# Optimization experiments

Measured on AMD Instinct MI355X. Metric: run time of the kernel, lower is better.

## Reference

```python
import jax, jax.numpy as jnp
import numpy as np

D_MODEL = 1024
NUM_HEADS = 16
HEAD_DIM = D_MODEL // NUM_HEADS  # 64
ROPE_THETA = 10000.0
BATCH = 2
SEQ = 2048
NEG_INF = -1e30


def setup_inputs() -> dict:
    key = jax.random.key(0)
    ks = jax.random.split(key, 6)
    std = 1.0 / np.sqrt(D_MODEL)
    x = jax.random.normal(ks[0], (BATCH, SEQ, D_MODEL), dtype=jnp.float32)
    wq = jax.random.normal(ks[1], (D_MODEL, D_MODEL), dtype=jnp.float32) * std
    wk = jax.random.normal(ks[2], (D_MODEL, D_MODEL), dtype=jnp.float32) * std
    wv = jax.random.normal(ks[3], (D_MODEL, D_MODEL), dtype=jnp.float32) * std
    wo = jax.random.normal(ks[4], (D_MODEL, D_MODEL), dtype=jnp.float32) * std
    token_positions = jnp.broadcast_to(jnp.arange(SEQ, dtype=jnp.int32)[None, :], (BATCH, SEQ))
    return {"x": x, "token_positions": token_positions, "wq": wq, "wk": wk, "wv": wv, "wo": wo}


def _apply_rope(t, token_positions):
    # t: (B, H, S, head_dim), token_positions: (B, S)
    half = HEAD_DIM // 2
    inv_freq = 1.0 / (ROPE_THETA ** (2.0 * jnp.arange(half, dtype=jnp.float32) / HEAD_DIM))
    angles = token_positions.astype(jnp.float32)[..., None] * inv_freq  # (B, S, half)
    cos = jnp.cos(angles)[:, None, :, :]  # (B, 1, S, half)
    sin = jnp.sin(angles)[:, None, :, :]
    tp = t.reshape(*t.shape[:-1], half, 2)  # interleaved pairs
    x1, x2 = tp[..., 0], tp[..., 1]
    r1 = x1 * cos - x2 * sin
    r2 = x1 * sin + x2 * cos
    return jnp.stack([r1, r2], axis=-1).reshape(t.shape)


def reference(x, token_positions, wq, wk, wv, wo):
    B, S, D = x.shape
    H, hd = NUM_HEADS, HEAD_DIM
    # projections (Linear: y = x @ W.T, no bias)
    q = (x @ wq.T).reshape(B, S, H, hd).transpose(0, 2, 1, 3)  # (B, H, S, hd)
    k = (x @ wk.T).reshape(B, S, H, hd).transpose(0, 2, 1, 3)
    v = (x @ wv.T).reshape(B, S, H, hd).transpose(0, 2, 1, 3)
    # RoPE on Q, K
    q = _apply_rope(q, token_positions)
    k = _apply_rope(k, token_positions)
    # causal scaled dot-product attention
    scores = jnp.einsum("bhqd,bhkd->bhqk", q, k) / jnp.sqrt(jnp.float32(hd))
    mask = jnp.tril(jnp.ones((S, S), dtype=bool))
    scores = jnp.where(mask, scores, NEG_INF)
    probs = jax.nn.softmax(scores, axis=-1)
    attn = jnp.einsum("bhqk,bhkd->bhqd", probs, v)  # (B, H, S, hd)
    attn = attn.transpose(0, 2, 1, 3).reshape(B, S, D)
    return attn @ wo.T
```

## Files before the change

kernel.cpp:

```cpp
#include <hip/hip_runtime.h>
#include <stdint.h>
#include <math.h>

#define SEQ 2048
#define NH 16
#define DM 1024

typedef __bf16 bf16x8 __attribute__((ext_vector_type(8)));
typedef float f32x4 __attribute__((ext_vector_type(4)));

__device__ __forceinline__ unsigned short f2bf(float f) {
  union { float f; unsigned u; } v; v.f = f;
  unsigned r = v.u + 0x7fffu + ((v.u >> 16) & 1u);
  return (unsigned short)(r >> 16);
}
__device__ __forceinline__ unsigned pk2(float a, float b) {
  return (unsigned)f2bf(a) | ((unsigned)f2bf(b) << 16);
}
__device__ __forceinline__ void load_lds16(const void* g, void* l) {
  __builtin_amdgcn_global_load_lds((__attribute__((address_space(1))) void*)g,
                                   (__attribute__((address_space(3))) void*)l,
                                   16, 0, 0);
}

__global__ void cvt_all(const float* __restrict__ x, const float* __restrict__ wq,
                        const float* __restrict__ wk, const float* __restrict__ wv,
                        const float* __restrict__ wo, unsigned short* __restrict__ ws) {
  const int i = blockIdx.x * blockDim.x + threadIdx.x;
  const int off = i * 4;
  const float* src;
  unsigned short* dst;
  if (off < 4194304) {
    src = x + off;  dst = ws + off;
  } else {
    const int r = off - 4194304;
    const int w = r >> 20, o = r & 1048575;
    const float* tabs[4] = {wq, wk, wv, wo};
    src = tabs[w] + o;  dst = ws + 4194304 + (w << 20) + o;
  }
  const float4 v = *(const float4*)src;
  ushort4 u;
  u.x = f2bf(v.x); u.y = f2bf(v.y); u.z = f2bf(v.z); u.w = f2bf(v.w);
  *(ushort4*)dst = u;
}

__launch_bounds__(256, 2)
__global__ void gemm_qkv(const unsigned short* __restrict__ X,
                         const unsigned short* __restrict__ W3,
                         unsigned short* __restrict__ Qr,
                         unsigned short* __restrict__ Kr,
                         unsigned short* __restrict__ Vt,
                         const int* __restrict__ tp) {
  __shared__ __align__(16) char smem[16384];
  char* As = smem;
  char* Bs = smem + 8192;

  const int t = threadIdx.x;
  const int lane = t & 63, wave = t >> 6;
  const int quad = lane >> 4, l16 = lane & 15;
  const int m0 = blockIdx.y * 128, n0 = blockIdx.x * 128;
  const int wm = (wave >> 1) * 64, wn = (wave & 1) * 64;

  f32x4 acc[4][4];
#pragma unroll
  for (int i = 0; i < 4; i++)
#pragma unroll
    for (int j = 0; j < 4; j++) { acc[i][j][0]=0.f; acc[i][j][1]=0.f; acc[i][j][2]=0.f; acc[i][j][3]=0.f; }

  const int rr = t >> 2;
  const int cc = (t & 3) * 8;

  for (int k0 = 0; k0 < 1024; k0 += 32) {
    __syncthreads();
#pragma unroll
    for (int i = 0; i < 2; i++) {
      load_lds16(X  + (uint64_t)(m0 + i * 64 + rr) * 1024 + k0 + cc, As + i * 4096 + wave * 1024);
      load_lds16(W3 + (uint64_t)(n0 + i * 64 + rr) * 1024 + k0 + cc, Bs + i * 4096 + wave * 1024);
    }
    __syncthreads();

    bf16x8 af[4], bfr[4];
#pragma unroll
    for (int i = 0; i < 4; i++) {
      af[i]  = *(const bf16x8*)(As + (wm + i * 16 + l16) * 64 + quad * 16);
      bfr[i] = *(const bf16x8*)(Bs + (wn + i * 16 + l16) * 64 + quad * 16);
    }
#pragma unroll
    for (int i = 0; i < 4; i++)
#pragma unroll
      for (int j = 0; j < 4; j++)
        acc[i][j] = __builtin_amdgcn_mfma_f32_16x16x32_bf16(af[i], bfr[j], acc[i][j], 0, 0, 0);
  }

  if (n0 < 2048) {
    unsigned short* dst = (n0 < 1024) ? Qr : Kr;
    float fr[4]; int dd[4], hh[4];
#pragma unroll
    for (int j = 0; j < 4; j++) {
      const int n = n0 + wn + j * 16 + l16;
      dd[j] = n & 63;
      hh[j] = (n & 1023) >> 6;
      fr[j] = __builtin_amdgcn_exp2f(-0.20762050594f * (float)(dd[j] & ~1)) * 0.15915494309f;
    }
    const float sgnodd = (l16 & 1) ? 1.f : -1.f;
#pragma unroll
    for (int i = 0; i < 4; i++) {
#pragma unroll
      for (int r = 0; r < 4; r++) {
        const int m = m0 + wm + i * 16 + quad * 4 + r;
        const int s = m & 2047, b = m >> 11;
        const float posf = (float)tp[m];
#pragma unroll
        for (int j = 0; j < 4; j++) {
          const float v = acc[i][j][r];
          const float p = __shfl_xor(v, 1);
          float rev = posf * fr[j];
          rev -= floorf(rev);
          float sn, cs;
          asm("v_sin_f32 %0, %1" : "=v"(sn) : "v"(rev));
          asm("v_cos_f32 %0, %1" : "=v"(cs) : "v"(rev));
          const float rv = fmaf(v, cs, p * sn * sgnodd);
          dst[((uint64_t)((b * NH + hh[j]) * SEQ + s)) * 64 + dd[j]] = f2bf(rv);
        }
      }
    }
  } else {
#pragma unroll
    for (int i = 0; i < 4; i++) {
      const int m = m0 + wm + i * 16 + quad * 4;
      const int s = m & 2047, b = m >> 11;
#pragma unroll
      for (int j = 0; j < 4; j++) {
        const int n = n0 - 2048 + wn + j * 16 + l16;
        const int h = n >> 6, d = n & 63;
        uint2 w;
        w.x = pk2(acc[i][j][0], acc[i][j][1]);
        w.y = pk2(acc[i][j][2], acc[i][j][3]);
        *(uint2*)(Vt + ((uint64_t)((b * NH + h) * 64 + d)) * SEQ + s) = w;
      }
    }
  }
}

__launch_bounds__(256, 2)
__global__ void gemm_ao(const unsigned short* __restrict__ A,
                        const unsigned short* __restrict__ B,
                        float* __restrict__ C) {
  __shared__ __align__(16) char smem[12288];
  char* As = smem;
  char* Bs = smem + 8192;

  const int t = threadIdx.x;
  const int lane = t & 63, wave = t >> 6;
  const int quad = lane >> 4, l16 = lane & 15;
  const int m0 = blockIdx.y * 128, n0 = blockIdx.x * 64;
  const int wm = (wave >> 1) * 64, wn = (wave & 1) * 32;

  f32x4 acc[4][2];
#pragma unroll
  for (int i = 0; i < 4; i++)
#pragma unroll
    for (int j = 0; j < 2; j++) { acc[i][j][0]=0.f; acc[i][j][1]=0.f; acc[i][j][2]=0.f; acc[i][j][3]=0.f; }

  const int rr = t >> 2;
  const int cc = (t & 3) * 8;

  for (int k0 = 0; k0 < 1024; k0 += 32) {
    __syncthreads();
#pragma unroll
    for (int i = 0; i < 2; i++)
      load_lds16(A + (uint64_t)(m0 + i * 64 + rr) * 1024 + k0 + cc, As + i * 4096 + wave * 1024);
    load_lds16(B + (uint64_t)(n0 + rr) * 1024 + k0 + cc, Bs + wave * 1024);
    __syncthreads();

    bf16x8 af[4], bfr[2];
#pragma unroll
    for (int i = 0; i < 4; i++)
      af[i] = *(const bf16x8*)(As + (wm + i * 16 + l16) * 64 + quad * 16);
#pragma unroll
    for (int j = 0; j < 2; j++)
      bfr[j] = *(const bf16x8*)(Bs + (wn + j * 16 + l16) * 64 + quad * 16);
#pragma unroll
    for (int i = 0; i < 4; i++)
#pragma unroll
      for (int j = 0; j < 2; j++)
        acc[i][j] = __builtin_amdgcn_mfma_f32_16x16x32_bf16(af[i], bfr[j], acc[i][j], 0, 0, 0);
  }

#pragma unroll
  for (int i = 0; i < 4; i++)
#pragma unroll
    for (int j = 0; j < 2; j++)
#pragma unroll
      for (int r = 0; r < 4; r++) {
        const int m = m0 + wm + i * 16 + quad * 4 + r;
        const int n = n0 + wn + j * 16 + l16;
        C[(uint64_t)m * DM + n] = acc[i][j][r];
      }
}

__launch_bounds__(256, 4)
__global__ void flash_attn(const unsigned short* __restrict__ Q,
                           const unsigned short* __restrict__ K,
                           const unsigned short* __restrict__ Vt,
                           unsigned short* __restrict__ Oa) {
  __shared__ __align__(16) char smem[40960];

  const int t = threadIdx.x;
  const int lane = t & 63, wave = t >> 6;
  const int quad = lane >> 4, l16 = lane & 15;
  const int bx = blockIdx.x;
  const int qt = (bx & 1) ? (31 - (bx >> 1)) : (bx >> 1);
  const int bh = blockIdx.y;
  const int qbase = qt * 64;
  const uint64_t base = (uint64_t)bh * (SEQ * 64);
  const int qg = qbase + wave * 16 + l16;

  bf16x8 qf[2];
  {
    const unsigned short* qp = Q + base + (uint64_t)qg * 64 + quad * 8;
    qf[0] = *(const bf16x8*)qp;
    qf[1] = *(const bf16x8*)(qp + 32);
  }

  f32x4 o[4];
#pragma unroll
  for (int i = 0; i < 4; i++) { o[i][0]=0.f; o[i][1]=0.f; o[i][2]=0.f; o[i][3]=0.f; }
  float mI = -1e30f, lI = 0.f;

  const int srow = wave * 8 + (lane >> 3);
  const int sc = ((lane & 7) ^ (lane >> 3)) * 8;
  const int swz = (l16 & 7);
  char* ps = smem + 32768 + wave * 2048;

#define STAGE(bufidx, kb_) do {                                                   \
    char* kd_ = smem + (bufidx) * 8192;                                           \
    char* vd_ = smem + 16384 + (bufidx) * 8192;                                   \
    _Pragma("unroll")                                                             \
    for (int i_ = 0; i_ < 2; i_++) {                                              \
      load_lds16(K  + base + (uint64_t)((kb_) + i_ * 32 + srow) * 64 + sc,        \
                 kd_ + i_ * 4096 + wave * 1024);                                  \
      load_lds16(Vt + base + (uint64_t)(i_ * 32 + srow) * SEQ + (kb_) + sc,       \
                 vd_ + i_ * 4096 + wave * 1024);                                  \
    }                                                                             \
  } while (0)

  STAGE(0, 0);

  for (int kt = 0; kt <= qt; kt++) {
    const int kb = kt * 64;
    const int buf = kt & 1;
    __syncthreads();
    if (kt < qt) STAGE(buf ^ 1, kb + 64);
    char* ks = smem + buf * 8192;
    char* vs = smem + 16384 + buf * 8192;
    const bool diag = (kt == qt);
    const int nbmax = diag ? (wave + 1) : 4;

    f32x4 sf[4];
#pragma unroll
    for (int nb = 0; nb < 4; nb++) {
      if (nb < nbmax) {
        f32x4 s; s[0]=0.f; s[1]=0.f; s[2]=0.f; s[3]=0.f;
#pragma unroll
        for (int kk = 0; kk < 2; kk++) {
          bf16x8 kfr = *(const bf16x8*)(ks + (nb * 16 + l16) * 128 + (((kk * 4 + quad) ^ swz) * 16));
          s = __builtin_amdgcn_mfma_f32_16x16x32_bf16(kfr, qf[kk], s, 0, 0, 0);
        }
        sf[nb] = s;
      } else {
        sf[nb][0] = -1e30f; sf[nb][1] = -1e30f; sf[nb][2] = -1e30f; sf[nb][3] = -1e30f;
      }
    }
    if (diag) {
#pragma unroll
      for (int nb = 0; nb < 4; nb++)
#pragma unroll
        for (int r = 0; r < 4; r++)
          if (kb + nb * 16 + quad * 4 + r > qg) sf[nb][r] = -1e30f;
    }

    float mx = sf[0][0];
#pragma unroll
    for (int nb = 0; nb < 4; nb++)
#pragma unroll
      for (int r = 0; r < 4; r++) mx = fmaxf(mx, sf[nb][r]);
    mx = fmaxf(mx, __shfl_xor(mx, 16));
    mx = fmaxf(mx, __shfl_xor(mx, 32));
    const float mnew = fmaxf(mI, mx);
    const float c1 = 0.18033688011f;
    const float mc = mnew * c1;
    const float alpha = __builtin_amdgcn_exp2f(mI * c1 - mc);
    mI = mnew;
    float ls = 0.f;
#pragma unroll
    for (int nb = 0; nb < 4; nb++)
#pragma unroll
      for (int r = 0; r < 4; r++) {
        const float p = __builtin_amdgcn_exp2f(sf[nb][r] * c1 - mc);
        sf[nb][r] = p;
        ls += p;
      }
    lI = lI * alpha + ls;
#pragma unroll
    for (int db = 0; db < 4; db++)
#pragma unroll
      for (int r = 0; r < 4; r++) o[db][r] *= alpha;

#pragma unroll
    for (int nb = 0; nb < 4; nb++) {
      uint2 pv;
      pv.x = pk2(sf[nb][0], sf[nb][1]);
      pv.y = pk2(sf[nb][2], sf[nb][3]);
      *(uint2*)(ps + l16 * 128 + (((nb * 2 + (quad >> 1)) ^ swz) * 16) + (quad & 1) * 8) = pv;
    }

    const int kkmax = diag ? ((wave >> 1) + 1) : 2;
    for (int kk = 0; kk < kkmax; kk++) {
      bf16x8 pf = *(const bf16x8*)(ps + l16 * 128 + (((kk * 4 + quad) ^ swz) * 16));
#pragma unroll
      for (int db = 0; db < 4; db++) {
        bf16x8 vf = *(const bf16x8*)(vs + (db * 16 + l16) * 128 + (((kk * 4 + quad) ^ swz) * 16));
        o[db] = __builtin_amdgcn_mfma_f32_16x16x32_bf16(vf, pf, o[db], 0, 0, 0);
      }
    }
  }
#undef STAGE

  lI += __shfl_xor(lI, 16);
  lI += __shfl_xor(lI, 32);
  const float invl = 1.0f / lI;
  const int b = bh >> 4, h = bh & 15;
  unsigned short* orow = Oa + ((uint64_t)(b * SEQ + qg)) * DM + h * 64 + quad * 4;
#pragma unroll
  for (int db = 0; db < 4; db++) {
    uint2 w;
    w.x = pk2(o[db][0] * invl, o[db][1] * invl);
    w.y = pk2(o[db][2] * invl, o[db][3] * invl);
    *(uint2*)(orow + db * 16) = w;
  }
}

extern "C" void kernel_launch(void* const* d_in, const int* in_sizes, int n_in,
                              void* d_out, int out_size, void* d_ws, size_t ws_size,
                              hipStream_t stream) {
  const float* x  = (const float*)d_in[0];
  const int* tp   = (const int*)d_in[1];
  const float* wq = (const float*)d_in[2];
  const float* wk = (const float*)d_in[3];
  const float* wv = (const float*)d_in[4];
  const float* wo = (const float*)d_in[5];
  float* out = (float*)d_out;

  unsigned short* ws = (unsigned short*)d_ws;
  unsigned short* xb  = ws;
  unsigned short* w3b = ws + 4194304;
  unsigned short* wob = ws + 7340032;
  unsigned short* Qr  = ws + 8388608;
  unsigned short* Kr  = ws + 12582912;
  unsigned short* Vt  = ws + 16777216;
  unsigned short* At  = ws + 20971520;

  cvt_all<<<8192, 256, 0, stream>>>(x, wq, wk, wv, wo, ws);
  gemm_qkv<<<dim3(24, 32), 256, 0, stream>>>(xb, w3b, Qr, Kr, Vt, tp);
  flash_attn<<<dim3(32, 32), 256, 0, stream>>>(Qr, Kr, Vt, At);
  gemm_ao<<<dim3(16, 32), 256, 0, stream>>>(At, wob, out);
}
```

Baseline: 206.5 us.

## Double-buffer LDS tiles in projection GEMMs and use raw waitcnt+barrier

Both GEMM kernels now use two LDS buffers so the async global-to-LDS load of the next K-slice is issued before computing on the current one, cutting the main loop to one barrier per iteration. The __syncthreads calls are replaced with an explicit s_waitcnt vmcnt(0) plus s_barrier, including in flash attention. This hides global load latency behind MFMA work. The cost is twice the LDS per block, which may lower occupancy, and correctness now depends on the hand-written waits covering the direct-to-LDS loads.

New measurement: 207.0 us. Within noise of the previous version (+0.3%).

```diff
diff --git a/kernel.cpp b/kernel.cpp
--- a/kernel.cpp
+++ b/kernel.cpp
@@ -8,6 +8,9 @@
 
 typedef __bf16 bf16x8 __attribute__((ext_vector_type(8)));
 typedef float f32x4 __attribute__((ext_vector_type(4)));
+
+#define ASM_VMCNT0  asm volatile("s_waitcnt vmcnt(0)" ::: "memory")
+#define ASM_BARRIER asm volatile("s_barrier" ::: "memory")
 
 __device__ __forceinline__ unsigned short f2bf(float f) {
   union { float f; unsigned u; } v; v.f = f;
@@ -51,9 +54,7 @@
                          unsigned short* __restrict__ Kr,
                          unsigned short* __restrict__ Vt,
                          const int* __restrict__ tp) {
-  __shared__ __align__(16) char smem[16384];
-  char* As = smem;
-  char* Bs = smem + 8192;
+  __shared__ __align__(16) char smem[32768];
 
   const int t = threadIdx.x;
   const int lane = t & 63, wave = t >> 6;
@@ -70,14 +71,27 @@
   const int rr = t >> 2;
   const int cc = (t & 3) * 8;
 
+#define QKV_STAGE(bufidx, k0_) do {                                               \
+    char* a_ = smem + (bufidx) * 8192;                                            \
+    char* b_ = smem + 16384 + (bufidx) * 8192;                                    \
+    _Pragma("unroll")                                                             \
+    for (int i_ = 0; i_ < 2; i_++) {                                              \
+      load_lds16(X  + (uint64_t)(m0 + i_ * 64 + rr) * 1024 + (k0_) + cc,          \
+                 a_ + i_ * 4096 + wave * 1024);                                   \
+      load_lds16(W3 + (uint64_t)(n0 + i_ * 64 + rr) * 1024 + (k0_) + cc,          \
+                 b_ + i_ * 4096 + wave * 1024);                                   \
+    }                                                                             \
+  } while (0)
+
+  QKV_STAGE(0, 0);
+
   for (int k0 = 0; k0 < 1024; k0 += 32) {
-    __syncthreads();
-#pragma unroll
-    for (int i = 0; i < 2; i++) {
-      load_lds16(X  + (uint64_t)(m0 + i * 64 + rr) * 1024 + k0 + cc, As + i * 4096 + wave * 1024);
-      load_lds16(W3 + (uint64_t)(n0 + i * 64 + rr) * 1024 + k0 + cc, Bs + i * 4096 + wave * 1024);
-    }
-    __syncthreads();
+    const int buf = (k0 >> 5) & 1;
+    ASM_VMCNT0;
+    ASM_BARRIER;
+    if (k0 + 32 < 1024) QKV_STAGE(buf ^ 1, k0 + 32);
+    char* As = smem + buf * 8192;
+    char* Bs = smem + 16384 + buf * 8192;
 
     bf16x8 af[4], bfr[4];
 #pragma unroll
@@ -91,6 +105,7 @@
       for (int j = 0; j < 4; j++)
         acc[i][j] = __builtin_amdgcn_mfma_f32_16x16x32_bf16(af[i], bfr[j], acc[i][j], 0, 0, 0);
   }
+#undef QKV_STAGE
 
   if (n0 < 2048) {
     unsigned short* dst = (n0 < 1024) ? Qr : Kr;
@@ -146,9 +161,7 @@
 __global__ void gemm_ao(const unsigned short* __restrict__ A,
                         const unsigned short* __restrict__ B,
                         float* __restrict__ C) {
-  __shared__ __align__(16) char smem[12288];
-  char* As = smem;
-  char* Bs = smem + 8192;
+  __shared__ __align__(16) char smem[24576];
 
   const int t = threadIdx.x;
   const int lane = t & 63, wave = t >> 6;
@@ -165,13 +178,25 @@
   const int rr = t >> 2;
   const int cc = (t & 3) * 8;
 
+#define AO_STAGE(bufidx, k0_) do {                                                \
+    char* a_ = smem + (bufidx) * 8192;                                            \
+    char* b_ = smem + 16384 + (bufidx) * 4096;                                    \
+    _Pragma("unroll")                                                             \
+    for (int i_ = 0; i_ < 2; i_++)                                                \
+      load_lds16(A + (uint64_t)(m0 + i_ * 64 + rr) * 1024 + (k0_) + cc,           \
+                 a_ + i_ * 4096 + wave * 1024);                                   \
+    load_lds16(B + (uint64_t)(n0 + rr) * 1024 + (k0_) + cc, b_ + wave * 1024);    \
+  } while (0)
+
+  AO_STAGE(0, 0);
+
   for (int k0 = 0; k0 < 1024; k0 += 32) {
-    __syncthreads();
-#pragma unroll
-    for (int i = 0; i < 2; i++)
-      load_lds16(A + (uint64_t)(m0 + i * 64 + rr) * 1024 + k0 + cc, As + i * 4096 + wave * 1024);
-    load_lds16(B + (uint64_t)(n0 + rr) * 1024 + k0 + cc, Bs + wave * 1024);
-    __syncthreads();
+    const int buf = (k0 >> 5) & 1;
+    ASM_VMCNT0;
+    ASM_BARRIER;
+    if (k0 + 32 < 1024) AO_STAGE(buf ^ 1, k0 + 32);
+    char* As = smem + buf * 8192;
+    char* Bs = smem + 16384 + buf * 4096;
 
     bf16x8 af[4], bfr[2];
 #pragma unroll
@@ -186,6 +211,7 @@
       for (int j = 0; j < 2; j++)
         acc[i][j] = __builtin_amdgcn_mfma_f32_16x16x32_bf16(af[i], bfr[j], acc[i][j], 0, 0, 0);
   }
+#undef AO_STAGE
 
 #pragma unroll
   for (int i = 0; i < 4; i++)
@@ -250,7 +276,8 @@
   for (int kt = 0; kt <= qt; kt++) {
     const int kb = kt * 64;
     const int buf = kt & 1;
-    __syncthreads();
+    ASM_VMCNT0;
+    ASM_BARRIER;
     if (kt < qt) STAGE(buf ^ 1, kb + 64);
     char* ks = smem + buf * 8192;
     char* vs = smem + 16384 + buf * 8192;
```
